# Optimization experiments

Hardware: AMD Instinct MI355X
Metric: run time of the kernel (lower is better)

Reference implementation:

```python
import jax, jax.numpy as jnp
import numpy as np

K, D = 512, 64


def setup_inputs() -> dict:
    key = jax.random.key(0)
    k1, k2 = jax.random.split(key)
    z_e_x = jax.random.normal(k1, (32, 4096, D), dtype=jnp.float32)
    # nn.Embedding weight initialized uniform(-1/K, 1/K)
    codebook = jax.random.uniform(k2, (K, D), dtype=jnp.float32,
                                  minval=-1.0 / K, maxval=1.0 / K)
    return {"z_e_x": z_e_x, "codebook": codebook}


def reference(z_e_x, codebook):
    # vq(): pairwise squared L2 distances to codebook, then argmin.
    d = z_e_x.shape[-1]
    flat = z_e_x.reshape(-1, d)                                   # [N, D]
    # ||z||^2 - 2 z.e + ||e||^2  (addmm form from original vq)
    dists = (jnp.sum(flat * flat, axis=1, keepdims=True)
             - 2.0 * flat @ codebook.T
             + jnp.sum(codebook * codebook, axis=1))              # [N, K]
    indices = jnp.argmin(dists, axis=1)                            # [N]
    # latents: indices reshaped to input shape minus feature dim
    return indices.reshape(z_e_x.shape[:-1])
```

## Files before the change

### kernel.cpp

```cpp
#include <hip/hip_runtime.h>
#include <math.h>

#define K_CODES 512
#define D_DIM   64
#define BM      128
#define NCHUNK  128
#define THREADS 256
#define LSTR    72
#define EPS_GAP 4e-5f

typedef __attribute__((ext_vector_type(8))) short short8v;
typedef __attribute__((ext_vector_type(4))) float f32x4;

__device__ __forceinline__ float np_sumsq64(const float* zarr) {
    float L[16];
#pragma unroll
    for (int j = 0; j < 16; ++j)
        L[j] = __fadd_rn(
            __fadd_rn(__fmul_rn(zarr[j],      zarr[j]),
                      __fmul_rn(zarr[j + 16], zarr[j + 16])),
            __fadd_rn(__fmul_rn(zarr[j + 32], zarr[j + 32]),
                      __fmul_rn(zarr[j + 48], zarr[j + 48])));
    float m[8];
#pragma unroll
    for (int j = 0; j < 8; ++j) m[j] = __fadd_rn(L[j], L[j + 8]);
    float n4[4];
#pragma unroll
    for (int j = 0; j < 4; ++j) n4[j] = __fadd_rn(m[j], m[j + 4]);
    return __fadd_rn(__fadd_rn(n4[0], n4[2]), __fadd_rn(n4[1], n4[3]));
}

__global__ __launch_bounds__(256) void vq_norms_kernel(const float* __restrict__ cb,
                                                       float* __restrict__ ws) {
    int k = blockIdx.x * blockDim.x + threadIdx.x;
    if (k == 0) reinterpret_cast<int*>(ws)[512] = 0;
    if (k >= K_CODES) return;
    float e[D_DIM];
    const float4* p = reinterpret_cast<const float4*>(cb + (size_t)k * D_DIM);
#pragma unroll
    for (int i = 0; i < 16; ++i) {
        float4 v = p[i];
        e[4*i+0]=v.x; e[4*i+1]=v.y; e[4*i+2]=v.z; e[4*i+3]=v.w;
    }
    ws[k] = np_sumsq64(e);
}

__device__ __forceinline__ unsigned short f32_bf16_rne(float x) {
    unsigned int u = __float_as_uint(x);
    unsigned int r = (u + 0x7FFFu + ((u >> 16) & 1u)) >> 16;
    return (unsigned short)r;
}
__device__ __forceinline__ float bf16_f32(unsigned short h) {
    return __uint_as_float(((unsigned int)h) << 16);
}
__device__ __forceinline__ void split2(float x, unsigned short& h, unsigned short& l) {
    h = f32_bf16_rne(x);
    l = f32_bf16_rne(x - bf16_f32(h));
}

__global__ __launch_bounds__(256)
void vq_pass1_kernel(const float* __restrict__ z, const float* __restrict__ cb,
                     const float* __restrict__ norms, int* __restrict__ out,
                     int* __restrict__ cnt, int* __restrict__ list, int cap, int n) {
    __shared__ unsigned short zhS[BM * LSTR];
    __shared__ unsigned short zlS[BM * LSTR];
    __shared__ unsigned short ehS[NCHUNK * LSTR];
    __shared__ unsigned short elS[NCHUNK * LSTR];
    __shared__ float nrmL[NCHUNK];

    const int tid  = threadIdx.x;
    const int l    = tid & 63;
    const int w    = tid >> 6;
    const int j    = l >> 4;
    const int c16  = l & 15;
    const int base = blockIdx.x * BM;

    const float4* z4 = reinterpret_cast<const float4*>(z);
#pragma unroll
    for (int rep = 0; rep < 8; ++rep) {
        int flat = rep * THREADS + tid;
        int pt   = flat >> 4;
        int dblk = flat & 15;
        int gp = base + pt; if (gp >= n) gp = n - 1;
        float4 v = z4[(size_t)gp * 16 + dblk];
        ushort4 h, lo;
        split2(v.x, h.x, lo.x); split2(v.y, h.y, lo.y);
        split2(v.z, h.z, lo.z); split2(v.w, h.w, lo.w);
        *reinterpret_cast<ushort4*>(&zhS[pt * LSTR + dblk * 4]) = h;
        *reinterpret_cast<ushort4*>(&zlS[pt * LSTR + dblk * 4]) = lo;
    }
    __syncthreads();

    short8v bzh[2][2], bzl[2][2];
#pragma unroll
    for (int p = 0; p < 2; ++p) {
        int pr = ((2 * w + p) * 16 + c16) * LSTR;
#pragma unroll
        for (int h = 0; h < 2; ++h) {
            int off = pr + h * 32 + j * 8;
            bzh[p][h] = *reinterpret_cast<const short8v*>(&zhS[off]);
            bzl[p][h] = *reinterpret_cast<const short8v*>(&zlS[off]);
        }
    }

    float m1[2] = {INFINITY, INFINITY};
    float m2[2] = {INFINITY, INFINITY};
    int   i1[2] = {0, 0};

    for (int c = 0; c < 4; ++c) {
        __syncthreads();
        const float4* cb4 = reinterpret_cast<const float4*>(cb);
#pragma unroll
        for (int rep = 0; rep < 8; ++rep) {
            int flat = rep * THREADS + tid;
            int code = flat >> 4;
            int dblk = flat & 15;
            float4 v = cb4[(size_t)(c * NCHUNK + code) * 16 + dblk];
            ushort4 h, lo;
            split2(v.x, h.x, lo.x); split2(v.y, h.y, lo.y);
            split2(v.z, h.z, lo.z); split2(v.w, h.w, lo.w);
            *reinterpret_cast<ushort4*>(&ehS[code * LSTR + dblk * 4]) = h;
            *reinterpret_cast<ushort4*>(&elS[code * LSTR + dblk * 4]) = lo;
        }
        if (tid < NCHUNK / 4)
            reinterpret_cast<float4*>(nrmL)[tid] =
                reinterpret_cast<const float4*>(norms)[c * (NCHUNK / 4) + tid];
        __syncthreads();

#pragma unroll
        for (int ct = 0; ct < 8; ++ct) {
            int ar = (ct * 16 + c16) * LSTR + j * 8;
            short8v aeh0 = *reinterpret_cast<const short8v*>(&ehS[ar]);
            short8v aeh1 = *reinterpret_cast<const short8v*>(&ehS[ar + 32]);
            short8v ael0 = *reinterpret_cast<const short8v*>(&elS[ar]);
            short8v ael1 = *reinterpret_cast<const short8v*>(&elS[ar + 32]);
            float4 nr = *reinterpret_cast<const float4*>(&nrmL[ct * 16 + j * 4]);
            float nra[4] = {nr.x, nr.y, nr.z, nr.w};
            int kg0 = c * NCHUNK + ct * 16 + j * 4;
#pragma unroll
            for (int p = 0; p < 2; ++p) {
                f32x4 acc = {0.f, 0.f, 0.f, 0.f};
                acc = __builtin_amdgcn_mfma_f32_16x16x32_bf16(aeh0, bzh[p][0], acc, 0, 0, 0);
                acc = __builtin_amdgcn_mfma_f32_16x16x32_bf16(aeh1, bzh[p][1], acc, 0, 0, 0);
                acc = __builtin_amdgcn_mfma_f32_16x16x32_bf16(aeh0, bzl[p][0], acc, 0, 0, 0);
                acc = __builtin_amdgcn_mfma_f32_16x16x32_bf16(aeh1, bzl[p][1], acc, 0, 0, 0);
                acc = __builtin_amdgcn_mfma_f32_16x16x32_bf16(ael0, bzh[p][0], acc, 0, 0, 0);
                acc = __builtin_amdgcn_mfma_f32_16x16x32_bf16(ael1, bzh[p][1], acc, 0, 0, 0);
#pragma unroll
                for (int r = 0; r < 4; ++r) {
                    float s = fmaf(-2.0f, acc[r], nra[r]);
                    int kg = kg0 + r;
                    bool lt1 = s < m1[p];
                    float nm2 = lt1 ? m1[p] : fminf(s, m2[p]);
                    i1[p] = lt1 ? kg : i1[p];
                    m1[p] = lt1 ? s : m1[p];
                    m2[p] = nm2;
                }
            }
        }
    }

#pragma unroll
    for (int p = 0; p < 2; ++p) {
        float a1 = m1[p], a2 = m2[p]; int ai = i1[p];
#pragma unroll
        for (int off = 16; off <= 32; off <<= 1) {
            float o1 = __shfl_xor(a1, off, 64);
            float o2 = __shfl_xor(a2, off, 64);
            int   oi = __shfl_xor(ai, off, 64);
            float hi = fmaxf(a1, o1);
            bool take = o1 < a1;
            ai = take ? oi : ai;
            a1 = take ? o1 : a1;
            a2 = fminf(hi, fminf(a2, o2));
        }
        int  ptg    = base + (2 * w + p) * 16 + c16;
        bool writer = (j == 0) && (ptg < n);
        bool flag   = writer && (a2 - a1 <= EPS_GAP);
        unsigned long long m = __ballot(flag);
        int abase = 0;
        if (m) {
            int leader = __ffsll(m) - 1;
            if (l == leader) abase = atomicAdd(cnt, __popcll(m));
            abase = __shfl(abase, leader, 64);
        }
        if (writer) {
            int val = ai;
            if (flag) {
                int rank = __popcll(m & ((1ull << l) - 1ull));
                int slot = abase + rank;
                if (slot < cap) list[slot] = ptg;
                else            val |= (int)0x80000000;
            }
            out[ptg] = val;
        }
    }
}

__device__ __forceinline__ void vq_rescan_point(
        const float* __restrict__ z, const float* __restrict__ cb,
        const float* __restrict__ norms, int* __restrict__ out,
        int pt, int lane) {
    float zr[D_DIM];
    const float4* zp = reinterpret_cast<const float4*>(z + (size_t)pt * D_DIM);
#pragma unroll
    for (int i = 0; i < 16; ++i) {
        float4 q = zp[i];
        zr[4*i+0]=q.x; zr[4*i+1]=q.y; zr[4*i+2]=q.z; zr[4*i+3]=q.w;
    }
    const float sz = np_sumsq64(zr);
    float best = INFINITY; int bi = 0x7FFFFFFF;
#pragma unroll 1
    for (int r = 0; r < 8; ++r) {
        const float4* e4 = reinterpret_cast<const float4*>(cb) +
                           ((size_t)(lane * 8 + r) << 4);
        float a = 0.f;
#pragma unroll
        for (int g = 0; g < 16; ++g) {
            float4 q = e4[g];
            a = fmaf(zr[4*g+0], q.x, a);
            a = fmaf(zr[4*g+1], q.y, a);
            a = fmaf(zr[4*g+2], q.z, a);
            a = fmaf(zr[4*g+3], q.w, a);
        }
        float s = __fadd_rn(__fsub_rn(sz, __fmul_rn(2.0f, a)),
                            norms[lane * 8 + r]);
        if (s < best) { best = s; bi = lane * 8 + r; }
    }
#pragma unroll
    for (int off = 1; off < 64; off <<= 1) {
        float os = __shfl_xor(best, off, 64);
        int   ok = __shfl_xor(bi, off, 64);
        if (os < best || (os == best && ok < bi)) { best = os; bi = ok; }
    }
    if (lane == 0) out[pt] = bi;
}

__global__ __launch_bounds__(256)
void vq_cleanup_kernel(const float* __restrict__ z, const float* __restrict__ cb,
                       const float* __restrict__ norms,
                       const int* __restrict__ cnt, const int* __restrict__ list,
                       int cap, int* __restrict__ out, int n) {
    const int lane   = threadIdx.x & 63;
    const int wid    = (blockIdx.x * blockDim.x + threadIdx.x) >> 6;
    const int nwaves = (gridDim.x * blockDim.x) >> 6;

    int total = *cnt;
    int lim   = total < cap ? total : cap;
    for (int i = wid; i < lim; i += nwaves)
        vq_rescan_point(z, cb, norms, out, list[i], lane);

    if (total > cap) {
        for (int b = wid * 64; b < n; b += nwaves * 64) {
            int t = b + lane;
            int v = (t < n) ? out[t] : 0;
            unsigned long long m = __ballot(v < 0);
            while (m) {
                int bb = __ffsll(m) - 1;
                m &= m - 1ull;
                vq_rescan_point(z, cb, norms, out, b + bb, lane);
            }
        }
    }
}

extern "C" void kernel_launch(void* const* d_in, const int* in_sizes, int n_in,
                              void* d_out, int out_size, void* d_ws, size_t ws_size,
                              hipStream_t stream) {
    const float* z  = (const float*)d_in[0];
    const float* cb = (const float*)d_in[1];
    int n = in_sizes[0] / D_DIM;
    float* norms = (float*)d_ws;
    int*   cnt   = (int*)d_ws + 512;
    int*   list  = (int*)d_ws + 513;
    int    cap   = (int)(ws_size / 4) - 513;
    if (cap < 0) cap = 0;
    int* out = (int*)d_out;

    vq_norms_kernel<<<(K_CODES + 255) / 256, 256, 0, stream>>>(cb, norms);
    vq_pass1_kernel<<<(n + BM - 1) / BM, THREADS, 0, stream>>>(z, cb, norms, out,
                                                               cnt, list, cap, n);
    vq_cleanup_kernel<<<512, 256, 0, stream>>>(z, cb, norms, cnt, list, cap, out, n);
}
```

Measured before the change: 67.61 us.

## Pre-split codebook into bf16 hi/lo once and stream via global_load_lds

A prep kernel now computes codebook norms and writes the bf16 hi/lo split of every code into workspace, padded to the LDS stride. The new pass-1 kernel keeps the split z fragments in registers instead of staging them in shared memory, and copies codebook chunks directly from global memory into LDS with global_load_lds. This removes the per-block codebook split and the z LDS staging, and lowers LDS use so more blocks can be resident. It needs a larger workspace and keeps the old path as a fallback when the workspace is too small.

```diff
diff --git a/kernel.cpp b/kernel.cpp
--- a/kernel.cpp
+++ b/kernel.cpp
@@ -9,6 +9,11 @@
 #define LSTR    72
 #define EPS_GAP 4e-5f
 
+#define WS_CNT_OFF  2048
+#define WS_EH_OFF   4096
+#define WS_EL_OFF   77824
+#define WS_LIST_OFF 151552
+
 typedef __attribute__((ext_vector_type(8))) short short8v;
 typedef __attribute__((ext_vector_type(4))) float f32x4;
 
@@ -30,21 +35,6 @@
     return __fadd_rn(__fadd_rn(n4[0], n4[2]), __fadd_rn(n4[1], n4[3]));
 }
 
-__global__ __launch_bounds__(256) void vq_norms_kernel(const float* __restrict__ cb,
-                                                       float* __restrict__ ws) {
-    int k = blockIdx.x * blockDim.x + threadIdx.x;
-    if (k == 0) reinterpret_cast<int*>(ws)[512] = 0;
-    if (k >= K_CODES) return;
-    float e[D_DIM];
-    const float4* p = reinterpret_cast<const float4*>(cb + (size_t)k * D_DIM);
-#pragma unroll
-    for (int i = 0; i < 16; ++i) {
-        float4 v = p[i];
-        e[4*i+0]=v.x; e[4*i+1]=v.y; e[4*i+2]=v.z; e[4*i+3]=v.w;
-    }
-    ws[k] = np_sumsq64(e);
-}
-
 __device__ __forceinline__ unsigned short f32_bf16_rne(float x) {
     unsigned int u = __float_as_uint(x);
     unsigned int r = (u + 0x7FFFu + ((u >> 16) & 1u)) >> 16;
@@ -59,7 +49,180 @@
 }
 
 __global__ __launch_bounds__(256)
-void vq_pass1_kernel(const float* __restrict__ z, const float* __restrict__ cb,
+void vq_prep_kernel(const float* __restrict__ cb, float* __restrict__ ws,
+                    int do_split) {
+    int k = blockIdx.x * blockDim.x + threadIdx.x;
+    if (k == 0) *reinterpret_cast<int*>((char*)ws + WS_CNT_OFF) = 0;
+    if (k >= K_CODES) return;
+    float e[D_DIM];
+    const float4* p = reinterpret_cast<const float4*>(cb + (size_t)k * D_DIM);
+#pragma unroll
+    for (int i = 0; i < 16; ++i) {
+        float4 v = p[i];
+        e[4*i+0]=v.x; e[4*i+1]=v.y; e[4*i+2]=v.z; e[4*i+3]=v.w;
+    }
+    ws[k] = np_sumsq64(e);
+    if (do_split) {
+        unsigned short* eh = reinterpret_cast<unsigned short*>((char*)ws + WS_EH_OFF)
+                             + (size_t)k * LSTR;
+        unsigned short* el = reinterpret_cast<unsigned short*>((char*)ws + WS_EL_OFF)
+                             + (size_t)k * LSTR;
+#pragma unroll
+        for (int i = 0; i < D_DIM; ++i) {
+            unsigned short h, l;
+            split2(e[i], h, l);
+            eh[i] = h; el[i] = l;
+        }
+#pragma unroll
+        for (int i = D_DIM; i < LSTR; ++i) { eh[i] = 0; el[i] = 0; }
+    }
+}
+
+__global__ __launch_bounds__(256)
+void vq_pass1_fast(const float* __restrict__ z,
+                   const unsigned short* __restrict__ eh_g,
+                   const unsigned short* __restrict__ el_g,
+                   const float* __restrict__ norms, int* __restrict__ out,
+                   int* __restrict__ cnt, int* __restrict__ list, int cap, int n) {
+    __shared__ __align__(16) unsigned short ehS[NCHUNK * LSTR];
+    __shared__ __align__(16) unsigned short elS[NCHUNK * LSTR];
+    __shared__ float nrmL[NCHUNK];
+
+    const int tid  = threadIdx.x;
+    const int l    = tid & 63;
+    const int w    = tid >> 6;
+    const int j    = l >> 4;
+    const int c16  = l & 15;
+    const int base = blockIdx.x * BM;
+
+    short8v bzh[2][2], bzl[2][2];
+#pragma unroll
+    for (int p = 0; p < 2; ++p) {
+        int row = base + (2 * w + p) * 16 + c16;
+        if (row >= n) row = n - 1;
+        const float* zp = z + (size_t)row * D_DIM + j * 8;
+#pragma unroll
+        for (int h = 0; h < 2; ++h) {
+            float4 v0 = *reinterpret_cast<const float4*>(zp + h * 32);
+            float4 v1 = *reinterpret_cast<const float4*>(zp + h * 32 + 4);
+            unsigned short hh[8], ll[8];
+            split2(v0.x, hh[0], ll[0]); split2(v0.y, hh[1], ll[1]);
+            split2(v0.z, hh[2], ll[2]); split2(v0.w, hh[3], ll[3]);
+            split2(v1.x, hh[4], ll[4]); split2(v1.y, hh[5], ll[5]);
+            split2(v1.z, hh[6], ll[6]); split2(v1.w, hh[7], ll[7]);
+            short8v th, tl;
+#pragma unroll
+            for (int i = 0; i < 8; ++i) { th[i] = (short)hh[i]; tl[i] = (short)ll[i]; }
+            bzh[p][h] = th; bzl[p][h] = tl;
+        }
+    }
+
+    float m1[2] = {INFINITY, INFINITY};
+    float m2[2] = {INFINITY, INFINITY};
+    int   i1[2] = {0, 0};
+
+    for (int c = 0; c < 4; ++c) {
+        __syncthreads();
+        {
+            const char* esrc = (const char*)eh_g + (size_t)c * (NCHUNK * LSTR * 2);
+            const char* lsrc = (const char*)el_g + (size_t)c * (NCHUNK * LSTR * 2);
+#pragma unroll
+            for (int r2 = 0; r2 < 4; ++r2) {
+                size_t off = ((size_t)tid + (size_t)r2 * 256) * 16;
+                __builtin_amdgcn_global_load_lds(
+                    (const __attribute__((address_space(1))) void*)(esrc + off),
+                    (__attribute__((address_space(3))) void*)((char*)ehS + off), 16, 0, 0);
+                __builtin_amdgcn_global_load_lds(
+                    (const __attribute__((address_space(1))) void*)(lsrc + off),
+                    (__attribute__((address_space(3))) void*)((char*)elS + off), 16, 0, 0);
+            }
+            if (tid < 128) {
+                size_t off = 16384 + (size_t)tid * 16;
+                __builtin_amdgcn_global_load_lds(
+                    (const __attribute__((address_space(1))) void*)(esrc + off),
+                    (__attribute__((address_space(3))) void*)((char*)ehS + off), 16, 0, 0);
+                __builtin_amdgcn_global_load_lds(
+                    (const __attribute__((address_space(1))) void*)(lsrc + off),
+                    (__attribute__((address_space(3))) void*)((char*)elS + off), 16, 0, 0);
+            }
+            if (tid < NCHUNK / 4)
+                reinterpret_cast<float4*>(nrmL)[tid] =
+                    reinterpret_cast<const float4*>(norms)[c * (NCHUNK / 4) + tid];
+        }
+        __syncthreads();
+
+#pragma unroll
+        for (int ct = 0; ct < 8; ++ct) {
+            int ar = (ct * 16 + c16) * LSTR + j * 8;
+            short8v aeh0 = *reinterpret_cast<const short8v*>(&ehS[ar]);
+            short8v aeh1 = *reinterpret_cast<const short8v*>(&ehS[ar + 32]);
+            short8v ael0 = *reinterpret_cast<const short8v*>(&elS[ar]);
+            short8v ael1 = *reinterpret_cast<const short8v*>(&elS[ar + 32]);
+            float4 nr = *reinterpret_cast<const float4*>(&nrmL[ct * 16 + j * 4]);
+            float nra[4] = {nr.x, nr.y, nr.z, nr.w};
+            int kg0 = c * NCHUNK + ct * 16 + j * 4;
+#pragma unroll
+            for (int p = 0; p < 2; ++p) {
+                f32x4 acc = {0.f, 0.f, 0.f, 0.f};
+                acc = __builtin_amdgcn_mfma_f32_16x16x32_bf16(aeh0, bzh[p][0], acc, 0, 0, 0);
+                acc = __builtin_amdgcn_mfma_f32_16x16x32_bf16(aeh1, bzh[p][1], acc, 0, 0, 0);
+                acc = __builtin_amdgcn_mfma_f32_16x16x32_bf16(aeh0, bzl[p][0], acc, 0, 0, 0);
+                acc = __builtin_amdgcn_mfma_f32_16x16x32_bf16(aeh1, bzl[p][1], acc, 0, 0, 0);
+                acc = __builtin_amdgcn_mfma_f32_16x16x32_bf16(ael0, bzh[p][0], acc, 0, 0, 0);
+                acc = __builtin_amdgcn_mfma_f32_16x16x32_bf16(ael1, bzh[p][1], acc, 0, 0, 0);
+#pragma unroll
+                for (int r = 0; r < 4; ++r) {
+                    float s = fmaf(-2.0f, acc[r], nra[r]);
+                    int kg = kg0 + r;
+                    bool lt1 = s < m1[p];
+                    float nm2 = lt1 ? m1[p] : fminf(s, m2[p]);
+                    i1[p] = lt1 ? kg : i1[p];
+                    m1[p] = lt1 ? s : m1[p];
+                    m2[p] = nm2;
+                }
+            }
+        }
+    }
+
+#pragma unroll
+    for (int p = 0; p < 2; ++p) {
+        float a1 = m1[p], a2 = m2[p]; int ai = i1[p];
+#pragma unroll
+        for (int off = 16; off <= 32; off <<= 1) {
+            float o1 = __shfl_xor(a1, off, 64);
+            float o2 = __shfl_xor(a2, off, 64);
+            int   oi = __shfl_xor(ai, off, 64);
+            float hi = fmaxf(a1, o1);
+            bool take = o1 < a1;
+            ai = take ? oi : ai;
+            a1 = take ? o1 : a1;
+            a2 = fminf(hi, fminf(a2, o2));
+        }
+        int  ptg    = base + (2 * w + p) * 16 + c16;
+        bool writer = (j == 0) && (ptg < n);
+        bool flag   = writer && (a2 - a1 <= EPS_GAP);
+        unsigned long long m = __ballot(flag);
+        int abase = 0;
+        if (m) {
+            int leader = __ffsll(m) - 1;
+            if (l == leader) abase = atomicAdd(cnt, __popcll(m));
+            abase = __shfl(abase, leader, 64);
+        }
+        if (writer) {
+            int val = ai;
+            if (flag) {
+                int rank = __popcll(m & ((1ull << l) - 1ull));
+                int slot = abase + rank;
+                if (slot < cap) list[slot] = ptg;
+                else            val |= (int)0x80000000;
+            }
+            out[ptg] = val;
+        }
+    }
+}
+
+__global__ __launch_bounds__(256)
+void vq_pass1_legacy(const float* __restrict__ z, const float* __restrict__ cb,
                      const float* __restrict__ norms, int* __restrict__ out,
                      int* __restrict__ cnt, int* __restrict__ list, int cap, int n) {
     __shared__ unsigned short zhS[BM * LSTR];
@@ -271,14 +434,25 @@
     const float* cb = (const float*)d_in[1];
     int n = in_sizes[0] / D_DIM;
     float* norms = (float*)d_ws;
-    int*   cnt   = (int*)d_ws + 512;
-    int*   list  = (int*)d_ws + 513;
-    int    cap   = (int)(ws_size / 4) - 513;
-    if (cap < 0) cap = 0;
+    int*   cnt   = (int*)((char*)d_ws + WS_CNT_OFF);
     int* out = (int*)d_out;
 
-    vq_norms_kernel<<<(K_CODES + 255) / 256, 256, 0, stream>>>(cb, norms);
-    vq_pass1_kernel<<<(n + BM - 1) / BM, THREADS, 0, stream>>>(z, cb, norms, out,
-                                                               cnt, list, cap, n);
-    vq_cleanup_kernel<<<512, 256, 0, stream>>>(z, cb, norms, cnt, list, cap, out, n);
-}
+    bool fast = ws_size >= (size_t)WS_LIST_OFF + 4096;
+    vq_prep_kernel<<<(K_CODES + 255) / 256, 256, 0, stream>>>(cb, norms, fast ? 1 : 0);
+
+    if (fast) {
+        const unsigned short* eh = (const unsigned short*)((char*)d_ws + WS_EH_OFF);
+        const unsigned short* el = (const unsigned short*)((char*)d_ws + WS_EL_OFF);
+        int* list = (int*)((char*)d_ws + WS_LIST_OFF);
+        int  cap  = (int)((ws_size - WS_LIST_OFF) / 4);
+        vq_pass1_fast<<<(n + BM - 1) / BM, THREADS, 0, stream>>>(
+            z, eh, el, norms, out, cnt, list, cap, n);
+        vq_cleanup_kernel<<<512, 256, 0, stream>>>(z, cb, norms, cnt, list, cap, out, n);
+    } else {
+        int* list = (int*)d_ws + 513;
+        int  cap  = (int)(ws_size / 4) - 513; if (cap < 0) cap = 0;
+        vq_pass1_legacy<<<(n + BM - 1) / BM, THREADS, 0, stream>>>(
+            z, cb, norms, out, cnt, list, cap, n);
+        vq_cleanup_kernel<<<512, 256, 0, stream>>>(z, cb, norms, cnt, list, cap, out, n);
+    }
+}
```

Result: faster. 63.09 us (-6.7%).
